# Optimization experiments

Measured on AMD Instinct MI355X. Metric: run time of the kernel, lower is better.

Reference implementation:

```python
import jax, jax.numpy as jnp
import numpy as np

H = 2048      # hidden_size
NH = 16       # num heads
HD = H // NH  # head_dim = 128


def setup_inputs() -> dict:
    key = jax.random.key(0)
    ks = jax.random.split(key, 5)
    x = jax.random.normal(ks[0], (2, 2048, H), dtype=jnp.float32)
    # qkv_proj: Linear(H, 3H) with bias; out_proj: Linear(H, H) with bias
    s = 1.0 / np.sqrt(H)
    w_qkv = jax.random.uniform(ks[1], (3 * H, H), jnp.float32, -s, s)
    b_qkv = jax.random.uniform(ks[2], (3 * H,), jnp.float32, -s, s)
    w_out = jax.random.uniform(ks[3], (H, H), jnp.float32, -s, s)
    b_out = jax.random.uniform(ks[4], (H,), jnp.float32, -s, s)
    return {"x": x, "w_qkv": w_qkv, "b_qkv": b_qkv, "w_out": w_out, "b_out": b_out}


def reference(x, w_qkv, b_qkv, w_out, b_out):
    b, s, _ = x.shape
    # fused QKV projection: [b, s, 3H]
    xqkv = jnp.einsum('bsh,oh->bso', x, w_qkv) + b_qkv
    xqkv = xqkv.reshape(b, s, 3, NH, HD)
    q = xqkv[:, :, 0].transpose(0, 2, 1, 3)  # [b, nh, s, hd]
    k = xqkv[:, :, 1].transpose(0, 2, 1, 3)
    v = xqkv[:, :, 2].transpose(0, 2, 1, 3)
    # non-causal SDPA (attn_mask=None, is_causal=False)
    scores = jnp.einsum('bhqd,bhkd->bhqk', q, k) / np.sqrt(HD).astype(np.float32)
    attn = jax.nn.softmax(scores, axis=-1)
    out = jnp.einsum('bhqk,bhkd->bhqd', attn, v)
    out = out.transpose(0, 2, 1, 3).reshape(b, s, NH * HD)
    return jnp.einsum('bsh,oh->bso', out, w_out) + b_out
```

## Files before the change

### kernel.cpp

```cpp
#include <hip/hip_runtime.h>
#include <hip/hip_bf16.h>


typedef __bf16 bf16x8 __attribute__((ext_vector_type(8)));
typedef float f32x4 __attribute__((ext_vector_type(4)));
typedef unsigned short ushort8_t __attribute__((ext_vector_type(8)));
typedef unsigned short ushort4_t __attribute__((ext_vector_type(4)));

__device__ __forceinline__ unsigned short f2bf(float f) {
  unsigned int u = __float_as_uint(f);
  u += 0x7fffu + ((u >> 16) & 1u);
  return (unsigned short)(u >> 16);
}

__device__ __forceinline__ unsigned int pk2bf(float lo, float hi) {
  unsigned int a = (__float_as_uint(lo) + 0x8000u) >> 16;
  unsigned int b = (__float_as_uint(hi) + 0x8000u) & 0xffff0000u;
  return a | b;
}

__device__ __forceinline__ float fexp2(float x) {
#if __has_builtin(__builtin_amdgcn_exp2f)
  return __builtin_amdgcn_exp2f(x);
#else
  return exp2f(x);
#endif
}

__device__ __forceinline__ f32x4 mfma16(bf16x8 a, bf16x8 b, f32x4 c) {
  return __builtin_amdgcn_mfma_f32_16x16x32_bf16(a, b, c, 0, 0, 0);
}

__device__ __forceinline__ void gload_lds16(const void* g, void* lds) {
  __builtin_amdgcn_global_load_lds(
      (const __attribute__((address_space(1))) unsigned int*)g,
      (__attribute__((address_space(3))) unsigned int*)lds, 16, 0, 0);
}

__global__ __launch_bounds__(256) void f32_to_bf16_k(const float* __restrict__ in,
                                                     unsigned short* __restrict__ out,
                                                     int n) {
  int i = (blockIdx.x * 256 + threadIdx.x) * 8;
  if (i >= n) return;
  float4 a = *(const float4*)(in + i);
  float4 b = *(const float4*)(in + i + 4);
  ushort8_t o;
  o[0] = f2bf(a.x); o[1] = f2bf(a.y); o[2] = f2bf(a.z); o[3] = f2bf(a.w);
  o[4] = f2bf(b.x); o[5] = f2bf(b.y); o[6] = f2bf(b.z); o[7] = f2bf(b.w);
  *(ushort8_t*)(out + i) = o;
}

template <int OUT_MODE>
__global__ __launch_bounds__(256) void gemm_nt(const unsigned short* __restrict__ A,
                                               const unsigned short* __restrict__ B,
                                               const float* __restrict__ bias,
                                               void* __restrict__ Cout,
                                               int Ns, int K) {
  __shared__ __attribute__((aligned(16))) unsigned short As[128 * 64];
  __shared__ __attribute__((aligned(16))) unsigned short Bs[128 * 64];
  const int tid = threadIdx.x;
  const int lane = tid & 63;
  const int wv = tid >> 6;
  const int wm = wv >> 1, wn = wv & 1;
  const int lr = lane & 15, lg = lane >> 4;
  const int m0 = blockIdx.y * 128, n0 = blockIdx.x * 128;

  f32x4 acc[4][4];
#pragma unroll
  for (int i = 0; i < 4; ++i)
#pragma unroll
    for (int j = 0; j < 4; ++j) acc[i][j] = (f32x4){0.f, 0.f, 0.f, 0.f};

  for (int kt = 0; kt < K; kt += 64) {
    __syncthreads();
#pragma unroll
    for (int i = 0; i < 4; ++i) {
      int c = i * 256 + tid;
      int r = c >> 3;
      int lc = (c & 7) ^ (r & 7);
      gload_lds16(A + (size_t)(m0 + r) * K + kt + lc * 8, &As[c * 8]);
      gload_lds16(B + (size_t)(n0 + r) * K + kt + lc * 8, &Bs[c * 8]);
    }
    __syncthreads();
#pragma unroll
    for (int kk = 0; kk < 64; kk += 32) {
      bf16x8 af[4], bf[4];
#pragma unroll
      for (int i = 0; i < 4; ++i) {
        int pcA = ((kk >> 3) + lg) ^ (lr & 7);
        af[i] = *(const bf16x8*)&As[(wm * 64 + i * 16 + lr) * 64 + pcA * 8];
        bf[i] = *(const bf16x8*)&Bs[(wn * 64 + i * 16 + lr) * 64 + pcA * 8];
      }
#pragma unroll
      for (int i = 0; i < 4; ++i)
#pragma unroll
        for (int j = 0; j < 4; ++j) acc[i][j] = mfma16(af[i], bf[j], acc[i][j]);
    }
  }

#pragma unroll
  for (int j = 0; j < 4; ++j) {
    int n = n0 + wn * 64 + j * 16 + lr;
    float bv = bias[n];
#pragma unroll
    for (int i = 0; i < 4; ++i) {
      int mbase = m0 + wm * 64 + i * 16 + lg * 4;
      if (OUT_MODE == 2) {
        int hh = n >> 7, dd = n & 127;
        int b = mbase >> 11, s = mbase & 2047;
        ushort4_t o4;
#pragma unroll
        for (int r = 0; r < 4; ++r) o4[r] = f2bf(acc[i][j][r] + bv);
        *(ushort4_t*)&((unsigned short*)Cout)[((size_t)((b * 16 + hh) * 128 + dd)) * 2048 + s] = o4;
      } else {
#pragma unroll
        for (int r = 0; r < 4; ++r) {
          float v = acc[i][j][r] + bv;
          if (OUT_MODE == 1)
            ((unsigned short*)Cout)[(size_t)(mbase + r) * Ns + n] = f2bf(v);
          else
            ((float*)Cout)[(size_t)(mbase + r) * Ns + n] = v;
        }
      }
    }
  }
}

__device__ __forceinline__ void stage_half256(const unsigned short* __restrict__ src,
                                              int K, unsigned short* lds, int half,
                                              int tid) {
#pragma unroll
  for (int j = 0; j < 2; ++j) {
    int c = half * 1024 + j * 512 + tid;
    int r = c >> 3;
    int lc = (c & 7) ^ (r & 7);
    gload_lds16(src + (size_t)r * K + lc * 8, &lds[c * 8]);
  }
}

__device__ __forceinline__ void phase256(const unsigned short* __restrict__ Ac,
                                         const unsigned short* __restrict__ Bc,
                                         int kk, int wm, int wn, int lr, int lg,
                                         f32x4 acc[8][4]) {
  bf16x8 a[8];
  bf16x8 bb[4];
  const int pc = ((kk >> 3) + lg) ^ (lr & 7);
#pragma unroll
  for (int i = 0; i < 8; ++i)
    a[i] = *(const bf16x8*)&Ac[(wm * 128 + i * 16 + lr) * 64 + pc * 8];
#pragma unroll
  for (int j = 0; j < 4; ++j)
    bb[j] = *(const bf16x8*)&Bc[(wn * 64 + j * 16 + lr) * 64 + pc * 8];
  __builtin_amdgcn_s_setprio(1);
#pragma unroll
  for (int i = 0; i < 8; ++i)
#pragma unroll
    for (int j = 0; j < 4; ++j) acc[i][j] = mfma16(a[i], bb[j], acc[i][j]);
  __builtin_amdgcn_s_setprio(0);
}

__global__ __launch_bounds__(512, 2) void gemm256_nt(const unsigned short* __restrict__ A,
                                                     const unsigned short* __restrict__ B,
                                                     const float* __restrict__ bias,
                                                     unsigned short* __restrict__ C,
                                                     int Ns, int K) {
  __shared__ __attribute__((aligned(16))) unsigned short As0[256 * 64];
  __shared__ __attribute__((aligned(16))) unsigned short As1[256 * 64];
  __shared__ __attribute__((aligned(16))) unsigned short Bs0[256 * 64];
  __shared__ __attribute__((aligned(16))) unsigned short Bs1[256 * 64];

  const int tid = threadIdx.x;
  const int lane = tid & 63;
  const int w = tid >> 6;
  const int wm = w >> 2, wn = w & 3;
  const int lr = lane & 15, lg = lane >> 4;
  const int m0 = blockIdx.y * 256, n0 = blockIdx.x * 256;

  const unsigned short* Abase = A + (size_t)m0 * K;
  const unsigned short* Bbase = B + (size_t)n0 * K;

  f32x4 acc[8][4];
#pragma unroll
  for (int i = 0; i < 8; ++i)
#pragma unroll
    for (int j = 0; j < 4; ++j) acc[i][j] = (f32x4){0.f, 0.f, 0.f, 0.f};

  unsigned short* Ac = As0;  unsigned short* An = As1;
  unsigned short* Bc = Bs0;  unsigned short* Bn = Bs1;

  stage_half256(Abase, K, Ac, 0, tid);
  stage_half256(Abase, K, Ac, 1, tid);
  stage_half256(Bbase, K, Bc, 0, tid);
  stage_half256(Bbase, K, Bc, 1, tid);

  const int nkt = K >> 6;
  for (int t = 0; t < nkt; ++t) {
    const int tn = (t + 1) & (nkt - 1);
    const unsigned short* Asrc = Abase + tn * 64;
    const unsigned short* Bsrc = Bbase + tn * 64;

    stage_half256(Asrc, K, An, 0, tid);
    stage_half256(Asrc, K, An, 1, tid);
    asm volatile("s_waitcnt vmcnt(4)" ::: "memory");
    __builtin_amdgcn_s_barrier();
    __builtin_amdgcn_sched_barrier(0);

    phase256(Ac, Bc, 0, wm, wn, lr, lg, acc);

    stage_half256(Bsrc, K, Bn, 0, tid);
    stage_half256(Bsrc, K, Bn, 1, tid);
    asm volatile("" ::: "memory");
    __builtin_amdgcn_s_barrier();
    __builtin_amdgcn_sched_barrier(0);

    phase256(Ac, Bc, 32, wm, wn, lr, lg, acc);

    asm volatile("" ::: "memory");
    __builtin_amdgcn_s_barrier();
    __builtin_amdgcn_sched_barrier(0);

    unsigned short* ta = Ac; Ac = An; An = ta;
    unsigned short* tb = Bc; Bc = Bn; Bn = tb;
  }

#pragma unroll
  for (int j = 0; j < 4; ++j) {
    int n = n0 + wn * 64 + j * 16 + lr;
    float bv = bias[n];
#pragma unroll
    for (int i = 0; i < 8; ++i) {
      int mbase = m0 + wm * 128 + i * 16 + lg * 4;
#pragma unroll
      for (int r = 0; r < 4; ++r)
        C[(size_t)(mbase + r) * Ns + n] = f2bf(acc[i][j][r] + bv);
    }
  }
}

__device__ __forceinline__ void stage_tiles(const unsigned short* __restrict__ qkv,
                                            const unsigned short* __restrict__ vbase,
                                            int b, int h, int t, int tid,
                                            unsigned short* KsB, unsigned short* VtB) {
  const int s0k = t * 64;
  const int krow = b * 2048 + s0k;
#pragma unroll
  for (int i = 0; i < 4; ++i) {
    int c = i * 256 + tid;
    int r = c >> 4;
    int lc = (c & 15) ^ (r & 15);
    gload_lds16(qkv + (size_t)(krow + r) * 6144 + 2048 + h * 128 + lc * 8, &KsB[c * 8]);
  }
#pragma unroll
  for (int i = 0; i < 4; ++i) {
    int c = i * 256 + tid;
    int r = c >> 3;
    int lc = (c & 7) ^ (r & 7);
    gload_lds16(vbase + (size_t)r * 2048 + s0k + lc * 8, &VtB[c * 8]);
  }
}

__global__ __launch_bounds__(256, 2) void flash_attn(const unsigned short* __restrict__ qkv,
                                                     const unsigned short* __restrict__ vT,
                                                     unsigned short* __restrict__ attnb) {
  __shared__ __attribute__((aligned(16))) unsigned short Ks0[64 * 128];
  __shared__ __attribute__((aligned(16))) unsigned short Ks1[64 * 128];
  __shared__ __attribute__((aligned(16))) unsigned short Vt0[128 * 64];
  __shared__ __attribute__((aligned(16))) unsigned short Vt1[128 * 64];

  const int tid = threadIdx.x;
  const int lane = tid & 63;
  const int w = tid >> 6;
  const int bh = blockIdx.y;
  const int b = bh >> 4, h = bh & 15;
  const int q0 = blockIdx.x * 128;
  const int lr = lane & 15, lg = lane >> 4;
  const float cs = 0.08838834764831845f * 1.44269504088896340f;

  const unsigned short* vbase = vT + (size_t)bh * 128 * 2048;

  bf16x8 qf[2][4];
#pragma unroll
  for (int g = 0; g < 2; ++g) {
    int m = b * 2048 + q0 + w * 32 + g * 16 + lr;
    const unsigned short* qrow = qkv + (size_t)m * 6144 + h * 128;
#pragma unroll
    for (int kb = 0; kb < 4; ++kb) qf[g][kb] = *(const bf16x8*)(qrow + kb * 32 + lg * 8);
  }

  float l_i[2] = {0.f, 0.f};
  f32x4 O[2][8];
#pragma unroll
  for (int g = 0; g < 2; ++g)
#pragma unroll
    for (int nb = 0; nb < 8; ++nb) O[g][nb] = (f32x4){0.f, 0.f, 0.f, 0.f};

  unsigned short* Kc = Ks0;  unsigned short* Kn = Ks1;
  unsigned short* Vc = Vt0;  unsigned short* Vn = Vt1;

  stage_tiles(qkv, vbase, b, h, 0, tid, Kc, Vc);

  for (int t = 0; t < 32; ++t) {
    __syncthreads();
    if (t + 1 < 32) stage_tiles(qkv, vbase, b, h, t + 1, tid, Kn, Vn);

    f32x4 sc[2][4];
#pragma unroll
    for (int g = 0; g < 2; ++g)
#pragma unroll
      for (int cb = 0; cb < 4; ++cb) sc[g][cb] = (f32x4){0.f, 0.f, 0.f, 0.f};
    __builtin_amdgcn_s_setprio(1);
#pragma unroll
    for (int cb = 0; cb < 4; ++cb) {
#pragma unroll
      for (int kb = 0; kb < 4; ++kb) {
        int pc = (kb * 4 + lg) ^ lr;
        bf16x8 kf = *(const bf16x8*)&Kc[(cb * 16 + lr) * 128 + pc * 8];
        sc[0][cb] = mfma16(kf, qf[0][kb], sc[0][cb]);
        sc[1][cb] = mfma16(kf, qf[1][kb], sc[1][cb]);
      }
    }
    __builtin_amdgcn_s_setprio(0);

    unsigned int pk[2][4][2];
#pragma unroll
    for (int g = 0; g < 2; ++g) {
      float rs = 0.f;
#pragma unroll
      for (int cb = 0; cb < 4; ++cb) {
        float p0 = fexp2(sc[g][cb][0] * cs);
        float p1 = fexp2(sc[g][cb][1] * cs);
        float p2 = fexp2(sc[g][cb][2] * cs);
        float p3 = fexp2(sc[g][cb][3] * cs);
        rs += (p0 + p1) + (p2 + p3);
        pk[g][cb][0] = pk2bf(p0, p1);
        pk[g][cb][1] = pk2bf(p2, p3);
      }
      rs += __shfl_xor(rs, 16, 64);
      rs += __shfl_xor(rs, 32, 64);
      l_i[g] += rs;
    }

#pragma unroll
    for (int kb2 = 0; kb2 < 2; ++kb2) {
      bf16x8 pf[2];
#pragma unroll
      for (int g = 0; g < 2; ++g) {
        unsigned int a0 = pk[g][2 * kb2 + 0][0];
        unsigned int b0 = pk[g][2 * kb2 + 1][0];
        unsigned int a1 = pk[g][2 * kb2 + 0][1];
        unsigned int b1 = pk[g][2 * kb2 + 1][1];
        asm("v_permlane32_swap_b32 %0, %1" : "+v"(a0), "+v"(b0));
        asm("v_permlane16_swap_b32 %0, %1" : "+v"(a0), "+v"(b0));
        asm("v_permlane32_swap_b32 %0, %1" : "+v"(a1), "+v"(b1));
        asm("v_permlane16_swap_b32 %0, %1" : "+v"(a1), "+v"(b1));
        uint4 u;
        u.x = a0; u.y = a1; u.z = b0; u.w = b1;
        pf[g] = *(bf16x8*)&u;
      }
      __builtin_amdgcn_s_setprio(1);
#pragma unroll
      for (int nb = 0; nb < 8; ++nb) {
        int pc = (kb2 * 4 + lg) ^ (lr & 7);
        bf16x8 vtf = *(const bf16x8*)&Vc[(nb * 16 + lr) * 64 + pc * 8];
        O[0][nb] = mfma16(vtf, pf[0], O[0][nb]);
        O[1][nb] = mfma16(vtf, pf[1], O[1][nb]);
      }
      __builtin_amdgcn_s_setprio(0);
    }

    unsigned short* tk = Kc; Kc = Kn; Kn = tk;
    unsigned short* tv = Vc; Vc = Vn; Vn = tv;
  }

#pragma unroll
  for (int g = 0; g < 2; ++g) {
    int m = b * 2048 + q0 + w * 32 + g * 16 + lr;
    float inv = 1.0f / l_i[g];
    unsigned short* orow = attnb + (size_t)m * 2048 + h * 128;
#pragma unroll
    for (int nb = 0; nb < 8; ++nb) {
      ushort4_t o4;
#pragma unroll
      for (int r = 0; r < 4; ++r) o4[r] = f2bf(O[g][nb][r] * inv);
      *(ushort4_t*)&orow[nb * 16 + lg * 4] = o4;
    }
  }
}

extern "C" void kernel_launch(void* const* d_in, const int* in_sizes, int n_in,
                              void* d_out, int out_size, void* d_ws, size_t ws_size,
                              hipStream_t stream) {
  const float* x = (const float*)d_in[0];
  const float* w_qkv = (const float*)d_in[1];
  const float* b_qkv = (const float*)d_in[2];
  const float* w_out = (const float*)d_in[3];
  const float* b_out = (const float*)d_in[4];
  float* out = (float*)d_out;

  char* ws = (char*)d_ws;
  unsigned short* xb = (unsigned short*)ws;
  unsigned short* attnb = xb;
  unsigned short* wqkvb = (unsigned short*)(ws + (16u << 20));
  unsigned short* woutb = wqkvb;
  unsigned short* qkvb = (unsigned short*)(ws + (40u << 20));
  unsigned short* vT = (unsigned short*)(ws + (88u << 20));

  f32_to_bf16_k<<<8388608 / 2048, 256, 0, stream>>>(x, xb, 8388608);
  f32_to_bf16_k<<<12582912 / 2048, 256, 0, stream>>>(w_qkv, wqkvb, 12582912);

  gemm256_nt<<<dim3(16, 16), 512, 0, stream>>>(xb, wqkvb, b_qkv, qkvb, 6144, 2048);
  gemm_nt<2><<<dim3(16, 32), 256, 0, stream>>>(xb, wqkvb + (size_t)4096 * 2048,
                                               b_qkv + 4096, vT, 2048, 2048);

  f32_to_bf16_k<<<4194304 / 2048, 256, 0, stream>>>(w_out, woutb, 4194304);

  flash_attn<<<dim3(16, 32), 256, 0, stream>>>(qkvb, vT, attnb);

  gemm_nt<0><<<dim3(16, 32), 256, 0, stream>>>(attnb, woutb, b_out, out, 2048, 2048);
}
```

Baseline: 397.1 us.

## Merge fp32-to-bf16 conversions into one launch and read K/V directly from global

All three fp32-to-bf16 conversions now run in a single kernel launch, with w_out given its own workspace region instead of sharing the w_qkv buffer. This removes two launches. Separately, the flash attention kernel drops its double-buffered LDS staging of K and V tiles, the per-tile barrier and the setprio hints, and loads MFMA operands straight from global memory. That cuts synchronisation and LDS traffic, but every wave now makes uncached, strided global loads, and each K/V tile is re-read by all four waves instead of being shared once through LDS.

```diff
diff --git a/kernel.cpp b/kernel.cpp
--- a/kernel.cpp
+++ b/kernel.cpp
@@ -37,17 +37,28 @@
       (__attribute__((address_space(3))) unsigned int*)lds, 16, 0, 0);
 }
 
-__global__ __launch_bounds__(256) void f32_to_bf16_k(const float* __restrict__ in,
-                                                     unsigned short* __restrict__ out,
-                                                     int n) {
+__global__ __launch_bounds__(256) void cvt_all_k(const float* __restrict__ x,
+                                                 const float* __restrict__ wqkv,
+                                                 const float* __restrict__ wout,
+                                                 unsigned short* __restrict__ xb,
+                                                 unsigned short* __restrict__ wqkvb,
+                                                 unsigned short* __restrict__ woutb) {
   int i = (blockIdx.x * 256 + threadIdx.x) * 8;
-  if (i >= n) return;
-  float4 a = *(const float4*)(in + i);
-  float4 b = *(const float4*)(in + i + 4);
+  const float* in;
+  unsigned short* out;
+  if (i < 8388608) {
+    in = x + i; out = xb + i;
+  } else if (i < 20971520) {
+    in = wqkv + (i - 8388608); out = wqkvb + (i - 8388608);
+  } else {
+    in = wout + (i - 20971520); out = woutb + (i - 20971520);
+  }
+  float4 a = *(const float4*)(in);
+  float4 b = *(const float4*)(in + 4);
   ushort8_t o;
   o[0] = f2bf(a.x); o[1] = f2bf(a.y); o[2] = f2bf(a.z); o[3] = f2bf(a.w);
   o[4] = f2bf(b.x); o[5] = f2bf(b.y); o[6] = f2bf(b.z); o[7] = f2bf(b.w);
-  *(ushort8_t*)(out + i) = o;
+  *(ushort8_t*)(out) = o;
 }
 
 template <int OUT_MODE>
@@ -237,36 +248,9 @@
   }
 }
 
-__device__ __forceinline__ void stage_tiles(const unsigned short* __restrict__ qkv,
-                                            const unsigned short* __restrict__ vbase,
-                                            int b, int h, int t, int tid,
-                                            unsigned short* KsB, unsigned short* VtB) {
-  const int s0k = t * 64;
-  const int krow = b * 2048 + s0k;
-#pragma unroll
-  for (int i = 0; i < 4; ++i) {
-    int c = i * 256 + tid;
-    int r = c >> 4;
-    int lc = (c & 15) ^ (r & 15);
-    gload_lds16(qkv + (size_t)(krow + r) * 6144 + 2048 + h * 128 + lc * 8, &KsB[c * 8]);
-  }
-#pragma unroll
-  for (int i = 0; i < 4; ++i) {
-    int c = i * 256 + tid;
-    int r = c >> 3;
-    int lc = (c & 7) ^ (r & 7);
-    gload_lds16(vbase + (size_t)r * 2048 + s0k + lc * 8, &VtB[c * 8]);
-  }
-}
-
 __global__ __launch_bounds__(256, 2) void flash_attn(const unsigned short* __restrict__ qkv,
                                                      const unsigned short* __restrict__ vT,
                                                      unsigned short* __restrict__ attnb) {
-  __shared__ __attribute__((aligned(16))) unsigned short Ks0[64 * 128];
-  __shared__ __attribute__((aligned(16))) unsigned short Ks1[64 * 128];
-  __shared__ __attribute__((aligned(16))) unsigned short Vt0[128 * 64];
-  __shared__ __attribute__((aligned(16))) unsigned short Vt1[128 * 64];
-
   const int tid = threadIdx.x;
   const int lane = tid & 63;
   const int w = tid >> 6;
@@ -277,6 +261,7 @@
   const float cs = 0.08838834764831845f * 1.44269504088896340f;
 
   const unsigned short* vbase = vT + (size_t)bh * 128 * 2048;
+  const unsigned short* kbase = qkv + (size_t)(b * 2048) * 6144 + 2048 + h * 128;
 
   bf16x8 qf[2][4];
 #pragma unroll
@@ -294,32 +279,24 @@
 #pragma unroll
     for (int nb = 0; nb < 8; ++nb) O[g][nb] = (f32x4){0.f, 0.f, 0.f, 0.f};
 
-  unsigned short* Kc = Ks0;  unsigned short* Kn = Ks1;
-  unsigned short* Vc = Vt0;  unsigned short* Vn = Vt1;
-
-  stage_tiles(qkv, vbase, b, h, 0, tid, Kc, Vc);
-
   for (int t = 0; t < 32; ++t) {
-    __syncthreads();
-    if (t + 1 < 32) stage_tiles(qkv, vbase, b, h, t + 1, tid, Kn, Vn);
+    const int s0k = t * 64;
 
     f32x4 sc[2][4];
 #pragma unroll
     for (int g = 0; g < 2; ++g)
 #pragma unroll
       for (int cb = 0; cb < 4; ++cb) sc[g][cb] = (f32x4){0.f, 0.f, 0.f, 0.f};
-    __builtin_amdgcn_s_setprio(1);
 #pragma unroll
     for (int cb = 0; cb < 4; ++cb) {
+      const unsigned short* krow = kbase + (size_t)(s0k + cb * 16 + lr) * 6144;
 #pragma unroll
       for (int kb = 0; kb < 4; ++kb) {
-        int pc = (kb * 4 + lg) ^ lr;
-        bf16x8 kf = *(const bf16x8*)&Kc[(cb * 16 + lr) * 128 + pc * 8];
+        bf16x8 kf = *(const bf16x8*)(krow + kb * 32 + lg * 8);
         sc[0][cb] = mfma16(kf, qf[0][kb], sc[0][cb]);
         sc[1][cb] = mfma16(kf, qf[1][kb], sc[1][cb]);
       }
     }
-    __builtin_amdgcn_s_setprio(0);
 
     unsigned int pk[2][4][2];
 #pragma unroll
@@ -357,19 +334,14 @@
         u.x = a0; u.y = a1; u.z = b0; u.w = b1;
         pf[g] = *(bf16x8*)&u;
       }
-      __builtin_amdgcn_s_setprio(1);
 #pragma unroll
       for (int nb = 0; nb < 8; ++nb) {
-        int pc = (kb2 * 4 + lg) ^ (lr & 7);
-        bf16x8 vtf = *(const bf16x8*)&Vc[(nb * 16 + lr) * 64 + pc * 8];
+        bf16x8 vtf = *(const bf16x8*)(vbase + (size_t)(nb * 16 + lr) * 2048 +
+                                      s0k + kb2 * 32 + lg * 8);
         O[0][nb] = mfma16(vtf, pf[0], O[0][nb]);
         O[1][nb] = mfma16(vtf, pf[1], O[1][nb]);
       }
-      __builtin_amdgcn_s_setprio(0);
-    }
-
-    unsigned short* tk = Kc; Kc = Kn; Kn = tk;
-    unsigned short* tv = Vc; Vc = Vn; Vn = tv;
+    }
   }
 
 #pragma unroll
@@ -401,19 +373,16 @@
   unsigned short* xb = (unsigned short*)ws;
   unsigned short* attnb = xb;
   unsigned short* wqkvb = (unsigned short*)(ws + (16u << 20));
-  unsigned short* woutb = wqkvb;
   unsigned short* qkvb = (unsigned short*)(ws + (40u << 20));
   unsigned short* vT = (unsigned short*)(ws + (88u << 20));
-
-  f32_to_bf16_k<<<8388608 / 2048, 256, 0, stream>>>(x, xb, 8388608);
-  f32_to_bf16_k<<<12582912 / 2048, 256, 0, stream>>>(w_qkv, wqkvb, 12582912);
+  unsigned short* woutb = (unsigned short*)(ws + (104ull << 20));
+
+  cvt_all_k<<<25165824 / 2048, 256, 0, stream>>>(x, w_qkv, w_out, xb, wqkvb, woutb);
 
   gemm256_nt<<<dim3(16, 16), 512, 0, stream>>>(xb, wqkvb, b_qkv, qkvb, 6144, 2048);
   gemm_nt<2><<<dim3(16, 32), 256, 0, stream>>>(xb, wqkvb + (size_t)4096 * 2048,
                                                b_qkv + 4096, vT, 2048, 2048);
 
-  f32_to_bf16_k<<<4194304 / 2048, 256, 0, stream>>>(w_out, woutb, 4194304);
-
   flash_attn<<<dim3(16, 32), 256, 0, stream>>>(qkvb, vT, attnb);
 
   gemm_nt<0><<<dim3(16, 32), 256, 0, stream>>>(attnb, woutb, b_out, out, 2048, 2048);
```

After: 596.2 us. 1.5x slower.
